# Performance work log

Measured on AMD Instinct MI355X. Metric: run time of the kernel, lower is better.

The kernel has to match this reference:

```python
import jax, jax.numpy as jnp
import numpy as np

N, E, D_IN, D_H, D_OUT = 100000, 1600000, 128, 128, 47
BN_EPS = 1e-5


def setup_inputs() -> dict:
    key = jax.random.key(0)
    ks = jax.random.split(key, 12)
    x = jax.random.normal(ks[0], (N, D_IN), dtype=jnp.float32)
    edge_index = jax.random.randint(ks[1], (2, E), 0, N, dtype=jnp.int64)
    s = 1.0 / np.sqrt(D_H)
    return {
        "x": x,
        "edge_index": edge_index,
        "W1": jax.random.normal(ks[2], (D_IN, D_H), dtype=jnp.float32) * s,
        "b1": jnp.zeros((D_H,), dtype=jnp.float32),
        "gamma": jax.random.uniform(ks[3], (D_H,), dtype=jnp.float32, minval=0.5, maxval=1.5),
        "beta": jax.random.normal(ks[4], (D_H,), dtype=jnp.float32) * 0.1,
        "mean": jax.random.normal(ks[5], (D_H,), dtype=jnp.float32) * 0.1,
        "var": jax.random.uniform(ks[6], (D_H,), dtype=jnp.float32, minval=0.5, maxval=1.5),
        "W2": jax.random.normal(ks[7], (D_H, D_H), dtype=jnp.float32) * s,
        "b2": jnp.zeros((D_H,), dtype=jnp.float32),
        "Wf": jax.random.normal(ks[8], (D_H, D_OUT), dtype=jnp.float32) * s,
        "bf": jnp.zeros((D_OUT,), dtype=jnp.float32),
    }


def gcn_conv(x, src, dst, W, b, n):
    # x' = x @ W, then symmetric-normalized aggregation with self-loops (PyG GCNConv).
    h = x @ W
    loops = jnp.arange(n, dtype=src.dtype)
    s = jnp.concatenate([src, loops])
    d = jnp.concatenate([dst, loops])
    deg = jax.ops.segment_sum(jnp.ones_like(d, dtype=h.dtype), d, num_segments=n)
    dinv = jnp.where(deg > 0, jax.lax.rsqrt(deg), 0.0)
    norm = dinv[s] * dinv[d]                      # [E+N]
    msg = h[s] * norm[:, None]                    # [E+N, D] gather
    out = jax.ops.segment_sum(msg, d, num_segments=n)  # scatter-add
    return out + b


def reference(x, edge_index, W1, b1, gamma, beta, mean, var, W2, b2, Wf, bf):
    n = x.shape[0]
    src, dst = edge_index[0], edge_index[1]
    # layer 1: GCNConv -> BatchNorm (eval) -> ReLU -> dropout (identity in eval)
    h1 = gcn_conv(x, src, dst, W1, b1, n)
    h1 = (h1 - mean) * jax.lax.rsqrt(var + BN_EPS) * gamma + beta
    h1 = jax.nn.relu(h1)
    # layer 2 (last conv, no BN/act)
    h2 = gcn_conv(h1, src, dst, W2, b2, n)
    # JumpingKnowledge max over layer outputs
    jk = jnp.maximum(h1, h2)
    logits = jk @ Wf + bf
    return jax.nn.log_softmax(logits, axis=1)
```

## Files before the change

kernel.cpp:

```cpp
#include <hip/hip_runtime.h>
#include <math.h>

#define DH 128
#define DOUT 47
#define BN_EPS 1e-5f

typedef __attribute__((ext_vector_type(8))) short short8;
typedef __attribute__((ext_vector_type(4))) float float4v;
typedef __attribute__((ext_vector_type(2))) float float2v;

__device__ __forceinline__ unsigned bf16_rne(float f) {
    unsigned u = __float_as_uint(f);
    return (u + 0x7fffu + ((u >> 16) & 1u)) >> 16;
}
__device__ __forceinline__ unsigned pack_bf2(float a, float b) {
    return (bf16_rne(a) & 0xffffu) | (bf16_rne(b) << 16);
}
__device__ __forceinline__ float2 unpack_bf2(unsigned u) {
    return make_float2(__uint_as_float(u << 16),
                       __uint_as_float(u & 0xffff0000u));
}


__global__ __launch_bounds__(256) void prep_k(const float* __restrict__ W1,
                                              const float* __restrict__ W2,
                                              unsigned* __restrict__ W1b,
                                              unsigned* __restrict__ W2b,
                                              int* __restrict__ counts8,
                                              unsigned* __restrict__ bufA, int n) {
    int tid = threadIdx.x;
    if (blockIdx.x >= 2) {
        int i4 = (blockIdx.x - 2) * 256 + tid;
        if (i4 < n * 2) *(int4*)(counts8 + (size_t)i4 * 4) = make_int4(0, 0, 0, 0);
        return;
    }
    const float* W = blockIdx.x ? W2 : W1;
    unsigned* Wb = blockIdx.x ? W2b : W1b;
    if (blockIdx.x == 0 && tid < 64) bufA[(size_t)n * 64 + tid] = 0;
    for (int p = tid; p < 128 * 32; p += 256) {
        int nn = p >> 5;
        int k0 = (p & 31) << 2;
        float f0 = W[(size_t)(k0 + 0) * 128 + nn];
        float f1 = W[(size_t)(k0 + 1) * 128 + nn];
        float f2 = W[(size_t)(k0 + 2) * 128 + nn];
        float f3 = W[(size_t)(k0 + 3) * 128 + nn];
        uint2 v;
        v.x = pack_bf2(f0, f1);
        v.y = pack_bf2(f2, f3);
        *(uint2*)(Wb + (size_t)nn * 64 + (k0 >> 1)) = v;
    }
}

__device__ __forceinline__ int xcc_id() {
    int x;
    asm volatile("s_getreg_b32 %0, hwreg(HW_REG_XCC_ID)" : "=s"(x));
    return x & 7;
}

__global__ __launch_bounds__(256) void fused_gc_k(
    const float* __restrict__ A, const unsigned* __restrict__ Wb,
    unsigned* __restrict__ Cb, int M,
    const int* __restrict__ dst, int* __restrict__ counts8,
    int* __restrict__ rank, int e, int gemmBlocks, int n) {
    __shared__ ushort Bl[128 * 136];
    int bid = blockIdx.x;
    int r3 = bid % 3;
    int q3 = bid / 3;
    int tid = threadIdx.x;

    if (r3 == 2) {
        int xcc = xcc_id();
        int* cnt = counts8 + (size_t)xcc * n;
        int tag = xcc << 24;
        int i0 = (q3 * 256 + tid) * 8;
#define CADD(d) ((int)__hip_atomic_fetch_add(&cnt[(d)], 1, __ATOMIC_RELAXED, \
                                             __HIP_MEMORY_SCOPE_WORKGROUP) | tag)
        if (i0 + 8 <= e) {
            int4 d4 = *(const int4*)(dst + i0);
            int4 e4 = *(const int4*)(dst + i0 + 4);
            int4 r4, s4;
            r4.x = CADD(d4.x);
            r4.y = CADD(d4.y);
            r4.z = CADD(d4.z);
            r4.w = CADD(d4.w);
            s4.x = CADD(e4.x);
            s4.y = CADD(e4.y);
            s4.z = CADD(e4.z);
            s4.w = CADD(e4.w);
            *(int4*)(rank + i0) = r4;
            *(int4*)(rank + i0 + 4) = s4;
        } else {
            for (int i = i0; i < e; i++) rank[i] = CADD(dst[i]);
        }
#undef CADD
        return;
    }

    int gIdx = q3 * 2 + r3;
    if (gIdx >= gemmBlocks) return;
    {
        unsigned* Bu = (unsigned*)Bl;
        for (int q = tid; q < 128 * 16; q += 256) {
            int row = q >> 4;
            int c = (q & 15) << 2;
            uint4 v = *(const uint4*)(Wb + (size_t)row * 64 + c);
            *(uint4*)(Bu + (size_t)row * 68 + c) = v;
        }
    }
    __syncthreads();

    int lane = tid & 63;
    int wv = tid >> 6;
    int quad = lane >> 4;
    int l15 = lane & 15;
    int r0 = gIdx * 64 + wv * 16;
    int mload = r0 + l15;
    if (mload > M - 1) mload = M - 1;
    const float* Ar = A + (size_t)mload * 128 + quad * 8;

    float4v acc[8];
#pragma unroll
    for (int t = 0; t < 8; t++) acc[t] = (float4v){0.f, 0.f, 0.f, 0.f};

    for (int kp = 0; kp < 4; ++kp) {
        float4 a0 = *(const float4*)(Ar + kp * 32);
        float4 a1 = *(const float4*)(Ar + kp * 32 + 4);
        float af[8] = {a0.x, a0.y, a0.z, a0.w, a1.x, a1.y, a1.z, a1.w};
        short8 av;
#pragma unroll
        for (int j = 0; j < 8; j++) av[j] = (short)bf16_rne(af[j]);
        int kb = kp * 32 + quad * 8;
#pragma unroll
        for (int nt = 0; nt < 8; nt++) {
            short8 b8 = *(const short8*)(&Bl[(size_t)(nt * 16 + l15) * 136 + kb]);
            acc[nt] = __builtin_amdgcn_mfma_f32_16x16x32_bf16(av, b8, acc[nt], 0, 0, 0);
        }
    }

    ushort* Cu = (ushort*)Cb;
#pragma unroll
    for (int r = 0; r < 4; r++) {
        int row = r0 + quad * 4 + r;
        if (row < M) {
#pragma unroll
            for (int nt = 0; nt < 8; nt++) {
                Cu[(size_t)row * 128 + nt * 16 + l15] =
                    (ushort)bf16_rne(acc[nt][r]);
            }
        }
    }
}

__global__ __launch_bounds__(256) void scan1_k(const int* __restrict__ counts8,
                                               int* __restrict__ offsets,
                                               int* __restrict__ blocksums, int n) {
    __shared__ int sd[256];
    int tid = threadIdx.x;
    int base = blockIdx.x * 1024 + tid * 4;
    int v[4];
#pragma unroll
    for (int j = 0; j < 4; j++) {
        int idx = base + j;
        int c = 0;
        if (idx < n) {
#pragma unroll
            for (int r = 0; r < 8; r++) c += counts8[(size_t)r * n + idx];
            c = (c + 7) & ~7;
        }
        v[j] = c;
    }
    int tsum = v[0] + v[1] + v[2] + v[3];
    sd[tid] = tsum;
    __syncthreads();
    for (int off = 1; off < 256; off <<= 1) {
        int x = (tid >= off) ? sd[tid - off] : 0;
        __syncthreads();
        sd[tid] += x;
        __syncthreads();
    }
    if (tid == 255) blocksums[blockIdx.x] = sd[255];
    int run = sd[tid] - tsum;
    if (base + 0 < n) offsets[base + 0] = run;  run += v[0];
    if (base + 1 < n) offsets[base + 1] = run;  run += v[1];
    if (base + 2 < n) offsets[base + 2] = run;  run += v[2];
    if (base + 3 < n) offsets[base + 3] = run;
}

__global__ __launch_bounds__(128) void scan2_k(int* __restrict__ blocksums, int nb,
                                               int* __restrict__ el, int n) {
    __shared__ int sd[128];
    int tid = threadIdx.x;
    int v = (tid < nb) ? blocksums[tid] : 0;
    sd[tid] = v;
    __syncthreads();
    for (int off = 1; off < 128; off <<= 1) {
        int x = (tid >= off) ? sd[tid - off] : 0;
        __syncthreads();
        sd[tid] += x;
        __syncthreads();
    }
    if (tid < nb) blocksums[tid] = sd[tid] - v;
    int total = sd[127];
    if (tid < 96) el[total + tid] = n;
}

__global__ void finalize_k(int* __restrict__ offsets,
                           float* __restrict__ dinv, int* __restrict__ counts8,
                           const int* __restrict__ blocksums,
                           int* __restrict__ base8,
                           int* __restrict__ el, int n) {
    int i = blockIdx.x * 256 + threadIdx.x;
    if (i >= n) return;
    int o = offsets[i] + blocksums[i >> 10];
    offsets[i] = o;
    int run = o;
#pragma unroll
    for (int r = 0; r < 8; r++) {
        base8[(size_t)i * 8 + r] = run;
        run += counts8[(size_t)r * n + i];
    }
    int c = run - o;
    counts8[i] = c;
    dinv[i] = rsqrtf((float)(c + 1));
    int cP = (c + 7) & ~7;
    for (int j = o + c; j < o + cP; ++j) el[j] = n;
}

__global__ __launch_bounds__(256) void scatter_k(const int* __restrict__ src,
                                                 const int* __restrict__ dst,
                                                 const int* __restrict__ rank,
                                                 const int* __restrict__ base8,
                                                 const float* __restrict__ dinv,
                                                 int* __restrict__ el, int e) {
    int i0 = (blockIdx.x * 256 + threadIdx.x) * 4;
    if (i0 + 4 <= e) {
        int4 s4 = *(const int4*)(src + i0);
        int4 d4 = *(const int4*)(dst + i0);
        int4 r4 = *(const int4*)(rank + i0);
        unsigned qx = (unsigned)(dinv[s4.x] * 32767.f + 0.5f);
        unsigned qy = (unsigned)(dinv[s4.y] * 32767.f + 0.5f);
        unsigned qz = (unsigned)(dinv[s4.z] * 32767.f + 0.5f);
        unsigned qw = (unsigned)(dinv[s4.w] * 32767.f + 0.5f);
        int ix = base8[(size_t)d4.x * 8 + (((unsigned)r4.x >> 24) & 7)] + (r4.x & 0xFFFFFF);
        int iy = base8[(size_t)d4.y * 8 + (((unsigned)r4.y >> 24) & 7)] + (r4.y & 0xFFFFFF);
        int iz = base8[(size_t)d4.z * 8 + (((unsigned)r4.z >> 24) & 7)] + (r4.z & 0xFFFFFF);
        int iw = base8[(size_t)d4.w * 8 + (((unsigned)r4.w >> 24) & 7)] + (r4.w & 0xFFFFFF);
        el[ix] = (int)((unsigned)s4.x | (qx << 17));
        el[iy] = (int)((unsigned)s4.y | (qy << 17));
        el[iz] = (int)((unsigned)s4.z | (qz << 17));
        el[iw] = (int)((unsigned)s4.w | (qw << 17));
    } else {
        for (int i = i0; i < e; i++) {
            unsigned q = (unsigned)(dinv[src[i]] * 32767.f + 0.5f);
            int rw = rank[i];
            int idx = base8[(size_t)dst[i] * 8 + (((unsigned)rw >> 24) & 7)] + (rw & 0xFFFFFF);
            el[idx] = (int)((unsigned)src[i] | (q << 17));
        }
    }
}

__global__ __launch_bounds__(256) void gemm_bf16_k(const unsigned* __restrict__ Ab,
                                                   const unsigned* __restrict__ Wb,
                                                   unsigned* __restrict__ Cb, int M) {
    __shared__ ushort Bl[128 * 136];
    int tid = threadIdx.x;
    {
        unsigned* Bu = (unsigned*)Bl;
        for (int q = tid; q < 128 * 16; q += 256) {
            int row = q >> 4;
            int c = (q & 15) << 2;
            uint4 v = *(const uint4*)(Wb + (size_t)row * 64 + c);
            *(uint4*)(Bu + (size_t)row * 68 + c) = v;
        }
    }
    __syncthreads();

    int lane = tid & 63;
    int wv = tid >> 6;
    int quad = lane >> 4;
    int l15 = lane & 15;
    int r0 = blockIdx.x * 64 + wv * 16;
    int mload = r0 + l15;
    if (mload > M - 1) mload = M - 1;
    const unsigned* Ar = Ab + (size_t)mload * 64 + quad * 4;

    float4v acc[8];
#pragma unroll
    for (int t = 0; t < 8; t++) acc[t] = (float4v){0.f, 0.f, 0.f, 0.f};

    for (int kp = 0; kp < 4; ++kp) {
        uint4 a4 = *(const uint4*)(Ar + kp * 16);
        short8 av;
        av[0] = (short)(a4.x & 0xffff); av[1] = (short)(a4.x >> 16);
        av[2] = (short)(a4.y & 0xffff); av[3] = (short)(a4.y >> 16);
        av[4] = (short)(a4.z & 0xffff); av[5] = (short)(a4.z >> 16);
        av[6] = (short)(a4.w & 0xffff); av[7] = (short)(a4.w >> 16);
        int kb = kp * 32 + quad * 8;
#pragma unroll
        for (int nt = 0; nt < 8; nt++) {
            short8 b8 = *(const short8*)(&Bl[(size_t)(nt * 16 + l15) * 136 + kb]);
            acc[nt] = __builtin_amdgcn_mfma_f32_16x16x32_bf16(av, b8, acc[nt], 0, 0, 0);
        }
    }

    ushort* Cu = (ushort*)Cb;
#pragma unroll
    for (int r = 0; r < 4; r++) {
        int row = r0 + quad * 4 + r;
        if (row < M) {
#pragma unroll
            for (int nt = 0; nt < 8; nt++) {
                Cu[(size_t)row * 128 + nt * 16 + l15] =
                    (ushort)bf16_rne(acc[nt][r]);
            }
        }
    }
}

__device__ __forceinline__ float4 agg_core(const uint2* __restrict__ Hu2,
                                           const int* __restrict__ el,
                                           int start, int cnt, int node,
                                           float dvn, int li, int half) {
    float2v a01 = {0.f, 0.f};
    float2v a23 = {0.f, 0.f};
    int groups = ((cnt + 7) & ~7) >> 3;
    if (groups > 0) {
        const int* p = el + start + half * 4;

#define EDGE(cu, rr) {                                                       \
        float qf = (float)((unsigned)(rr) >> 17) * (1.f / 32767.f);          \
        float2v f0, f1;                                                      \
        f0.x = __uint_as_float((cu).x << 16);                                \
        f0.y = __uint_as_float((cu).x & 0xffff0000u);                        \
        f1.x = __uint_as_float((cu).y << 16);                                \
        f1.y = __uint_as_float((cu).y & 0xffff0000u);                        \
        a01.x = fmaf(f0.x, qf, a01.x); a01.y = fmaf(f0.y, qf, a01.y);        \
        a23.x = fmaf(f1.x, qf, a23.x); a23.y = fmaf(f1.y, qf, a23.y);        \
}
        int4 rc = *(const int4*)p;
        uint2 c0 = Hu2[(size_t)(rc.x & 0x1FFFF) * 32 + li];
        uint2 c1 = Hu2[(size_t)(rc.y & 0x1FFFF) * 32 + li];
        uint2 c2 = Hu2[(size_t)(rc.z & 0x1FFFF) * 32 + li];
        uint2 c3 = Hu2[(size_t)(rc.w & 0x1FFFF) * 32 + li];
        int4 rn = *(const int4*)(p + 8);
        for (int g = 0; g < groups; ++g) {
            uint2 n0 = Hu2[(size_t)(rn.x & 0x1FFFF) * 32 + li];
            uint2 n1 = Hu2[(size_t)(rn.y & 0x1FFFF) * 32 + li];
            uint2 n2 = Hu2[(size_t)(rn.z & 0x1FFFF) * 32 + li];
            uint2 n3 = Hu2[(size_t)(rn.w & 0x1FFFF) * 32 + li];
            int4 r2 = *(const int4*)(p + 8 * (g + 2));
            EDGE(c0, rc.x) EDGE(c1, rc.y) EDGE(c2, rc.z) EDGE(c3, rc.w)
            c0 = n0; c1 = n1; c2 = n2; c3 = n3;
            rc = rn; rn = r2;
        }
#undef EDGE
    }
    float4 acc = make_float4(a01.x, a01.y, a23.x, a23.y);
    acc.x += __shfl_xor(acc.x, 32);
    acc.y += __shfl_xor(acc.y, 32);
    acc.z += __shfl_xor(acc.z, 32);
    acc.w += __shfl_xor(acc.w, 32);
    uint2 sv = Hu2[(size_t)node * 32 + li];
    float2 s0 = unpack_bf2(sv.x);
    float2 s1 = unpack_bf2(sv.y);
    acc.x = fmaf(s0.x, dvn, acc.x); acc.y = fmaf(s0.y, dvn, acc.y);
    acc.z = fmaf(s1.x, dvn, acc.z); acc.w = fmaf(s1.y, dvn, acc.w);
    return acc;
}

__global__ __launch_bounds__(256) void agg1_k(
    const unsigned* __restrict__ H, const int* __restrict__ el,
    const int* __restrict__ offsets, const int* __restrict__ counts,
    const float* __restrict__ dinv, const float* __restrict__ b1,
    const float* __restrict__ gamma, const float* __restrict__ beta,
    const float* __restrict__ mean, const float* __restrict__ var,
    unsigned* __restrict__ H1b, int n) {
    int lane = threadIdx.x & 63;
    int li = lane & 31;
    int half = lane >> 5;
    int node = blockIdx.x * 4 + (threadIdx.x >> 6);
    if (node >= n) return;
    float dv = dinv[node];
    float4 acc = agg_core((const uint2*)H, el, offsets[node],
                          counts[node], node, dv, li, half);
    if (half == 0) {
        int f0 = li * 4;
        float4 bb = *(const float4*)(b1 + f0);
        float4 mm = *(const float4*)(mean + f0);
        float4 vv = *(const float4*)(var + f0);
        float4 gg = *(const float4*)(gamma + f0);
        float4 be = *(const float4*)(beta + f0);
        float4 o;
        o.x = fmaxf((acc.x * dv + bb.x - mm.x) * rsqrtf(vv.x + BN_EPS) * gg.x + be.x, 0.f);
        o.y = fmaxf((acc.y * dv + bb.y - mm.y) * rsqrtf(vv.y + BN_EPS) * gg.y + be.y, 0.f);
        o.z = fmaxf((acc.z * dv + bb.z - mm.z) * rsqrtf(vv.z + BN_EPS) * gg.z + be.z, 0.f);
        o.w = fmaxf((acc.w * dv + bb.w - mm.w) * rsqrtf(vv.w + BN_EPS) * gg.w + be.w, 0.f);
        uint2 pk;
        pk.x = pack_bf2(o.x, o.y);
        pk.y = pack_bf2(o.z, o.w);
        *(uint2*)(H1b + (size_t)node * 64 + li * 2) = pk;
    }
}

__global__ __launch_bounds__(256) void agg2_k(
    const unsigned* __restrict__ H, const int* __restrict__ el,
    const int* __restrict__ offsets, const int* __restrict__ counts,
    const float* __restrict__ dinv, const float* __restrict__ b2,
    unsigned* __restrict__ H1b, int n) {
    int lane = threadIdx.x & 63;
    int li = lane & 31;
    int half = lane >> 5;
    int node = blockIdx.x * 4 + (threadIdx.x >> 6);
    if (node >= n) return;
    float dv = dinv[node];
    float4 acc = agg_core((const uint2*)H, el, offsets[node],
                          counts[node], node, dv, li, half);
    if (half == 0) {
        int f0 = li * 4;
        float4 bb = *(const float4*)(b2 + f0);
        uint2* p = (uint2*)(H1b + (size_t)node * 64 + li * 2);
        uint2 hv = *p;
        float2 ha = unpack_bf2(hv.x);
        float2 hb = unpack_bf2(hv.y);
        float4 o;
        o.x = fmaxf(ha.x, acc.x * dv + bb.x);
        o.y = fmaxf(ha.y, acc.y * dv + bb.y);
        o.z = fmaxf(hb.x, acc.z * dv + bb.z);
        o.w = fmaxf(hb.y, acc.w * dv + bb.w);
        uint2 pk;
        pk.x = pack_bf2(o.x, o.y);
        pk.y = pack_bf2(o.z, o.w);
        *p = pk;
    }
}

__global__ __launch_bounds__(256) void head_k(const unsigned* __restrict__ JKb,
                                              const float* __restrict__ Wf,
                                              const float* __restrict__ bf,
                                              float* __restrict__ out, int n) {
    __shared__ __align__(16) float Bs[48 * 132];
    __shared__ __align__(16) float As[64 * 36];
    int tid = threadIdx.x;
    for (int p = tid; p < 47 * 32; p += 256) {
        int c = p >> 5;
        int k0 = (p & 31) << 2;
        float4 v;
        v.x = Wf[(size_t)(k0 + 0) * DOUT + c];
        v.y = Wf[(size_t)(k0 + 1) * DOUT + c];
        v.z = Wf[(size_t)(k0 + 2) * DOUT + c];
        v.w = Wf[(size_t)(k0 + 3) * DOUT + c];
        *(float4*)(&Bs[c * 132 + k0]) = v;
    }
    int tx = tid & 15;
    int ty = tid >> 4;
    int node0 = blockIdx.x * 64;

    float acc[4][3];
#pragma unroll
    for (int i = 0; i < 4; i++)
#pragma unroll
        for (int j = 0; j < 3; j++) acc[i][j] = 0.f;

    for (int kk = 0; kk < 128; kk += 32) {
        __syncthreads();
        for (int l = tid; l < 512; l += 256) {
            int r = l >> 3;
            int c4 = (l & 7) << 2;
            int row = node0 + r;
            float4 v = make_float4(0.f, 0.f, 0.f, 0.f);
            if (row < n) {
                uint2 u = *(const uint2*)(JKb + (size_t)row * 64 + ((kk + c4) >> 1));
                float2 f0 = unpack_bf2(u.x);
                float2 f1 = unpack_bf2(u.y);
                v = make_float4(f0.x, f0.y, f1.x, f1.y);
            }
            *(float4*)(&As[r * 36 + c4]) = v;
        }
        __syncthreads();
#pragma unroll
        for (int k4 = 0; k4 < 32; k4 += 4) {
            float4 a0 = *(const float4*)(&As[(ty * 4 + 0) * 36 + k4]);
            float4 a1 = *(const float4*)(&As[(ty * 4 + 1) * 36 + k4]);
            float4 a2 = *(const float4*)(&As[(ty * 4 + 2) * 36 + k4]);
            float4 a3 = *(const float4*)(&As[(ty * 4 + 3) * 36 + k4]);
            float4 b0 = *(const float4*)(&Bs[(tx * 3 + 0) * 132 + kk + k4]);
            float4 b1 = *(const float4*)(&Bs[(tx * 3 + 1) * 132 + kk + k4]);
            float4 b2 = *(const float4*)(&Bs[(tx * 3 + 2) * 132 + kk + k4]);
#define DOT_ROW(i, a)                                                        \
            acc[i][0] = fmaf(a.x, b0.x, acc[i][0]);                          \
            acc[i][0] = fmaf(a.y, b0.y, acc[i][0]);                          \
            acc[i][0] = fmaf(a.z, b0.z, acc[i][0]);                          \
            acc[i][0] = fmaf(a.w, b0.w, acc[i][0]);                          \
            acc[i][1] = fmaf(a.x, b1.x, acc[i][1]);                          \
            acc[i][1] = fmaf(a.y, b1.y, acc[i][1]);                          \
            acc[i][1] = fmaf(a.z, b1.z, acc[i][1]);                          \
            acc[i][1] = fmaf(a.w, b1.w, acc[i][1]);                          \
            acc[i][2] = fmaf(a.x, b2.x, acc[i][2]);                          \
            acc[i][2] = fmaf(a.y, b2.y, acc[i][2]);                          \
            acc[i][2] = fmaf(a.z, b2.z, acc[i][2]);                          \
            acc[i][2] = fmaf(a.w, b2.w, acc[i][2]);
            DOT_ROW(0, a0)
            DOT_ROW(1, a1)
            DOT_ROW(2, a2)
            DOT_ROW(3, a3)
#undef DOT_ROW
        }
    }

    float bfv[3];
#pragma unroll
    for (int j = 0; j < 3; j++) {
        int c = tx * 3 + j;
        bfv[j] = (c < DOUT) ? bf[c] : 0.f;
    }
#pragma unroll
    for (int i = 0; i < 4; i++) {
        int node = node0 + ty * 4 + i;
        float l0 = acc[i][0] + bfv[0];
        float l1 = acc[i][1] + bfv[1];
        float l2 = acc[i][2] + bfv[2];
        bool v2ok = (tx * 3 + 2) < DOUT;
        float m = fmaxf(l0, l1);
        if (v2ok) m = fmaxf(m, l2);
        for (int off = 8; off >= 1; off >>= 1) m = fmaxf(m, __shfl_xor(m, off));
        float s = expf(l0 - m) + expf(l1 - m) + (v2ok ? expf(l2 - m) : 0.f);
        for (int off = 8; off >= 1; off >>= 1) s += __shfl_xor(s, off);
        float ls = m + logf(s);
        if (node < n) {
            float* o = out + (size_t)node * DOUT + tx * 3;
            o[0] = l0 - ls;
            o[1] = l1 - ls;
            if (v2ok) o[2] = l2 - ls;
        }
    }
}

extern "C" void kernel_launch(void* const* d_in, const int* in_sizes, int n_in,
                              void* d_out, int out_size, void* d_ws, size_t ws_size,
                              hipStream_t stream) {
    const float* x     = (const float*)d_in[0];
    const int*   ei    = (const int*)d_in[1];
    const float* W1    = (const float*)d_in[2];
    const float* b1    = (const float*)d_in[3];
    const float* gamma = (const float*)d_in[4];
    const float* beta  = (const float*)d_in[5];
    const float* mean  = (const float*)d_in[6];
    const float* var   = (const float*)d_in[7];
    const float* W2    = (const float*)d_in[8];
    const float* b2    = (const float*)d_in[9];
    const float* Wf    = (const float*)d_in[10];
    const float* bf    = (const float*)d_in[11];
    float* out = (float*)d_out;

    int N_ = in_sizes[0] / 128;
    int E_ = in_sizes[1] / 2;
    const int* src = ei;
    const int* dst = ei + E_;

    char* ws = (char*)d_ws;
    unsigned* bufA = (unsigned*)ws; ws += (size_t)(N_ + 1) * 64 * 4;
    unsigned* h1b  = (unsigned*)ws; ws += (size_t)N_ * 64 * 4;
    int* counts8   = (int*)ws;    ws += (size_t)N_ * 8 * 4;
    int* base8     = (int*)ws;    ws += (size_t)N_ * 8 * 4;
    int*   offsets = (int*)ws;    ws += (size_t)N_ * 4;
    float* dinv    = (float*)ws;  ws += (size_t)N_ * 4;
    int*   rank    = (int*)ws;    ws += (size_t)E_ * 4;
    int*   el      = (int*)ws;    ws += ((size_t)E_ + 7 * (size_t)N_ + 128) * 4;
    int*   bsums   = (int*)ws;    ws += 1024 * 4;
    unsigned* W1b  = (unsigned*)ws; ws += 128 * 64 * 4;
    unsigned* W2b  = (unsigned*)ws; ws += 128 * 64 * 4;

    int nb = (N_ + 1023) / 1024;
    int gemmBlocks = (N_ + 63) / 64;
    int countBlocks = (E_ + 2047) / 2048;
    int pairs = countBlocks > (gemmBlocks + 1) / 2 ? countBlocks : (gemmBlocks + 1) / 2;
    int fusedGrid = 3 * pairs;
    int edgeBlocks = (E_ + 1023) / 1024;
    int zeroBlocks = (N_ * 2 + 255) / 256;

    prep_k<<<2 + zeroBlocks, 256, 0, stream>>>(W1, W2, W1b, W2b, counts8, bufA, N_);
    fused_gc_k<<<fusedGrid, 256, 0, stream>>>(x, W1b, bufA, N_,
                                              dst, counts8, rank, E_, gemmBlocks, N_);
    scan1_k<<<nb, 256, 0, stream>>>(counts8, offsets, bsums, N_);
    scan2_k<<<1, 128, 0, stream>>>(bsums, nb, el, N_);
    finalize_k<<<(N_ + 255) / 256, 256, 0, stream>>>(offsets, dinv,
                                                     counts8, bsums, base8, el, N_);
    scatter_k<<<edgeBlocks, 256, 0, stream>>>(src, dst, rank, base8, dinv, el, E_);

    agg1_k<<<(N_ + 3) / 4, 256, 0, stream>>>(bufA, el, offsets, counts8, dinv,
                                             b1, gamma, beta, mean, var, h1b, N_);
    gemm_bf16_k<<<gemmBlocks, 256, 0, stream>>>(h1b, W2b, bufA, N_);
    agg2_k<<<(N_ + 3) / 4, 256, 0, stream>>>(bufA, el, offsets, counts8, dinv,
                                             b2, h1b, N_);
    head_k<<<(N_ + 63) / 64, 256, 0, stream>>>(h1b, Wf, bf, out, N_);
}
```

Baseline: 420.4 us.

## Replace global atomic degree counting with LDS-bin chunked histogram and fuse scatter with GEMM

Degree counting and per-edge ranking now run in a dedicated kernel that keeps a 32K-node range of bins in shared memory for each of 64 edge chunks, using LDS atomics instead of per-XCC global atomics. Per-chunk counts are reduced in the scan and turned into per-chunk base offsets in finalize, with the per-chunk count buffer aliased onto the h1 buffer. The first feature GEMM is moved out of the counting kernel and fused with the edge scatter kernel. This trades global atomic traffic for one more read pass over dst per node range and a larger 64-way reduction in scan and finalize.

```diff
diff --git a/kernel.cpp b/kernel.cpp
--- a/kernel.cpp
+++ b/kernel.cpp
@@ -4,6 +4,10 @@
 #define DH 128
 #define DOUT 47
 #define BN_EPS 1e-5f
+
+#define NCH 64
+#define RS 32768
+#define RSH 15
 
 typedef __attribute__((ext_vector_type(8))) short short8;
 typedef __attribute__((ext_vector_type(4))) float float4v;
@@ -26,14 +30,8 @@
                                               const float* __restrict__ W2,
                                               unsigned* __restrict__ W1b,
                                               unsigned* __restrict__ W2b,
-                                              int* __restrict__ counts8,
                                               unsigned* __restrict__ bufA, int n) {
     int tid = threadIdx.x;
-    if (blockIdx.x >= 2) {
-        int i4 = (blockIdx.x - 2) * 256 + tid;
-        if (i4 < n * 2) *(int4*)(counts8 + (size_t)i4 * 4) = make_int4(0, 0, 0, 0);
-        return;
-    }
     const float* W = blockIdx.x ? W2 : W1;
     unsigned* Wb = blockIdx.x ? W2b : W1b;
     if (blockIdx.x == 0 && tid < 64) bufA[(size_t)n * 64 + tid] = 0;
@@ -51,109 +49,51 @@
     }
 }
 
-__device__ __forceinline__ int xcc_id() {
-    int x;
-    asm volatile("s_getreg_b32 %0, hwreg(HW_REG_XCC_ID)" : "=s"(x));
-    return x & 7;
-}
-
-__global__ __launch_bounds__(256) void fused_gc_k(
-    const float* __restrict__ A, const unsigned* __restrict__ Wb,
-    unsigned* __restrict__ Cb, int M,
-    const int* __restrict__ dst, int* __restrict__ counts8,
-    int* __restrict__ rank, int e, int gemmBlocks, int n) {
-    __shared__ ushort Bl[128 * 136];
-    int bid = blockIdx.x;
-    int r3 = bid % 3;
-    int q3 = bid / 3;
-    int tid = threadIdx.x;
-
-    if (r3 == 2) {
-        int xcc = xcc_id();
-        int* cnt = counts8 + (size_t)xcc * n;
-        int tag = xcc << 24;
-        int i0 = (q3 * 256 + tid) * 8;
-#define CADD(d) ((int)__hip_atomic_fetch_add(&cnt[(d)], 1, __ATOMIC_RELAXED, \
-                                             __HIP_MEMORY_SCOPE_WORKGROUP) | tag)
-        if (i0 + 8 <= e) {
+__global__ __launch_bounds__(256) void hist_rank_k(const int* __restrict__ dst,
+                                                   int* __restrict__ rank,
+                                                   int* __restrict__ cntM,
+                                                   int e, int ce, int nr,
+                                                   size_t nsp) {
+    __shared__ int bins[RS];
+    int tid = threadIdx.x;
+    int r = blockIdx.x % nr;
+    int ch = blockIdx.x / nr;
+    {
+        int4* b4 = (int4*)bins;
+        for (int j = tid; j < RS / 4; j += 256) b4[j] = make_int4(0, 0, 0, 0);
+    }
+    __syncthreads();
+    int lo = ch * ce;
+    int hi = lo + ce;
+    if (hi > e) hi = e;
+    if (lo < hi) {
+        int n4end = lo + ((hi - lo) & ~3);
+        for (int i0 = lo + tid * 4; i0 < n4end; i0 += 1024) {
             int4 d4 = *(const int4*)(dst + i0);
-            int4 e4 = *(const int4*)(dst + i0 + 4);
-            int4 r4, s4;
-            r4.x = CADD(d4.x);
-            r4.y = CADD(d4.y);
-            r4.z = CADD(d4.z);
-            r4.w = CADD(d4.w);
-            s4.x = CADD(e4.x);
-            s4.y = CADD(e4.y);
-            s4.z = CADD(e4.z);
-            s4.w = CADD(e4.w);
-            *(int4*)(rank + i0) = r4;
-            *(int4*)(rank + i0 + 4) = s4;
-        } else {
-            for (int i = i0; i < e; i++) rank[i] = CADD(dst[i]);
-        }
-#undef CADD
-        return;
-    }
-
-    int gIdx = q3 * 2 + r3;
-    if (gIdx >= gemmBlocks) return;
+            if ((d4.x >> RSH) == r) rank[i0 + 0] = atomicAdd(&bins[d4.x & (RS - 1)], 1);
+            if ((d4.y >> RSH) == r) rank[i0 + 1] = atomicAdd(&bins[d4.y & (RS - 1)], 1);
+            if ((d4.z >> RSH) == r) rank[i0 + 2] = atomicAdd(&bins[d4.z & (RS - 1)], 1);
+            if ((d4.w >> RSH) == r) rank[i0 + 3] = atomicAdd(&bins[d4.w & (RS - 1)], 1);
+        }
+        for (int i0 = n4end + tid; i0 < hi; i0 += 256) {
+            int d = dst[i0];
+            if ((d >> RSH) == r) rank[i0] = atomicAdd(&bins[d & (RS - 1)], 1);
+        }
+    }
+    __syncthreads();
     {
-        unsigned* Bu = (unsigned*)Bl;
-        for (int q = tid; q < 128 * 16; q += 256) {
-            int row = q >> 4;
-            int c = (q & 15) << 2;
-            uint4 v = *(const uint4*)(Wb + (size_t)row * 64 + c);
-            *(uint4*)(Bu + (size_t)row * 68 + c) = v;
-        }
-    }
-    __syncthreads();
-
-    int lane = tid & 63;
-    int wv = tid >> 6;
-    int quad = lane >> 4;
-    int l15 = lane & 15;
-    int r0 = gIdx * 64 + wv * 16;
-    int mload = r0 + l15;
-    if (mload > M - 1) mload = M - 1;
-    const float* Ar = A + (size_t)mload * 128 + quad * 8;
-
-    float4v acc[8];
-#pragma unroll
-    for (int t = 0; t < 8; t++) acc[t] = (float4v){0.f, 0.f, 0.f, 0.f};
-
-    for (int kp = 0; kp < 4; ++kp) {
-        float4 a0 = *(const float4*)(Ar + kp * 32);
-        float4 a1 = *(const float4*)(Ar + kp * 32 + 4);
-        float af[8] = {a0.x, a0.y, a0.z, a0.w, a1.x, a1.y, a1.z, a1.w};
-        short8 av;
-#pragma unroll
-        for (int j = 0; j < 8; j++) av[j] = (short)bf16_rne(af[j]);
-        int kb = kp * 32 + quad * 8;
-#pragma unroll
-        for (int nt = 0; nt < 8; nt++) {
-            short8 b8 = *(const short8*)(&Bl[(size_t)(nt * 16 + l15) * 136 + kb]);
-            acc[nt] = __builtin_amdgcn_mfma_f32_16x16x32_bf16(av, b8, acc[nt], 0, 0, 0);
-        }
-    }
-
-    ushort* Cu = (ushort*)Cb;
-#pragma unroll
-    for (int r = 0; r < 4; r++) {
-        int row = r0 + quad * 4 + r;
-        if (row < M) {
-#pragma unroll
-            for (int nt = 0; nt < 8; nt++) {
-                Cu[(size_t)row * 128 + nt * 16 + l15] =
-                    (ushort)bf16_rne(acc[nt][r]);
-            }
-        }
-    }
-}
-
-__global__ __launch_bounds__(256) void scan1_k(const int* __restrict__ counts8,
+        int* outp = cntM + (size_t)ch * nsp + ((size_t)r << RSH);
+        const int4* b4 = (const int4*)bins;
+        int4* o4 = (int4*)outp;
+        for (int j = tid; j < RS / 4; j += 256) o4[j] = b4[j];
+    }
+}
+
+__global__ __launch_bounds__(256) void scan1_k(const int* __restrict__ cntM,
+                                               int* __restrict__ counts,
                                                int* __restrict__ offsets,
-                                               int* __restrict__ blocksums, int n) {
+                                               int* __restrict__ blocksums,
+                                               size_t nsp, int n) {
     __shared__ int sd[256];
     int tid = threadIdx.x;
     int base = blockIdx.x * 1024 + tid * 4;
@@ -163,8 +103,8 @@
         int idx = base + j;
         int c = 0;
         if (idx < n) {
-#pragma unroll
-            for (int r = 0; r < 8; r++) c += counts8[(size_t)r * n + idx];
+            for (int ch = 0; ch < NCH; ch++) c += cntM[(size_t)ch * nsp + idx];
+            counts[idx] = c;
             c = (c + 7) & ~7;
         }
         v[j] = c;
@@ -205,56 +145,115 @@
 }
 
 __global__ void finalize_k(int* __restrict__ offsets,
-                           float* __restrict__ dinv, int* __restrict__ counts8,
+                           float* __restrict__ dinv,
+                           const int* __restrict__ counts,
                            const int* __restrict__ blocksums,
-                           int* __restrict__ base8,
-                           int* __restrict__ el, int n) {
+                           int* __restrict__ cntM,
+                           int* __restrict__ el, size_t nsp, int n) {
     int i = blockIdx.x * 256 + threadIdx.x;
     if (i >= n) return;
     int o = offsets[i] + blocksums[i >> 10];
     offsets[i] = o;
     int run = o;
-#pragma unroll
-    for (int r = 0; r < 8; r++) {
-        base8[(size_t)i * 8 + r] = run;
-        run += counts8[(size_t)r * n + i];
-    }
-    int c = run - o;
-    counts8[i] = c;
+    for (int ch = 0; ch < NCH; ch++) {
+        size_t idx = (size_t)ch * nsp + i;
+        int c = cntM[idx];
+        cntM[idx] = run;
+        run += c;
+    }
+    int c = counts[i];
     dinv[i] = rsqrtf((float)(c + 1));
     int cP = (c + 7) & ~7;
     for (int j = o + c; j < o + cP; ++j) el[j] = n;
 }
 
-__global__ __launch_bounds__(256) void scatter_k(const int* __restrict__ src,
-                                                 const int* __restrict__ dst,
-                                                 const int* __restrict__ rank,
-                                                 const int* __restrict__ base8,
-                                                 const float* __restrict__ dinv,
-                                                 int* __restrict__ el, int e) {
-    int i0 = (blockIdx.x * 256 + threadIdx.x) * 4;
-    if (i0 + 4 <= e) {
-        int4 s4 = *(const int4*)(src + i0);
-        int4 d4 = *(const int4*)(dst + i0);
-        int4 r4 = *(const int4*)(rank + i0);
-        unsigned qx = (unsigned)(dinv[s4.x] * 32767.f + 0.5f);
-        unsigned qy = (unsigned)(dinv[s4.y] * 32767.f + 0.5f);
-        unsigned qz = (unsigned)(dinv[s4.z] * 32767.f + 0.5f);
-        unsigned qw = (unsigned)(dinv[s4.w] * 32767.f + 0.5f);
-        int ix = base8[(size_t)d4.x * 8 + (((unsigned)r4.x >> 24) & 7)] + (r4.x & 0xFFFFFF);
-        int iy = base8[(size_t)d4.y * 8 + (((unsigned)r4.y >> 24) & 7)] + (r4.y & 0xFFFFFF);
-        int iz = base8[(size_t)d4.z * 8 + (((unsigned)r4.z >> 24) & 7)] + (r4.z & 0xFFFFFF);
-        int iw = base8[(size_t)d4.w * 8 + (((unsigned)r4.w >> 24) & 7)] + (r4.w & 0xFFFFFF);
-        el[ix] = (int)((unsigned)s4.x | (qx << 17));
-        el[iy] = (int)((unsigned)s4.y | (qy << 17));
-        el[iz] = (int)((unsigned)s4.z | (qz << 17));
-        el[iw] = (int)((unsigned)s4.w | (qw << 17));
-    } else {
-        for (int i = i0; i < e; i++) {
-            unsigned q = (unsigned)(dinv[src[i]] * 32767.f + 0.5f);
-            int rw = rank[i];
-            int idx = base8[(size_t)dst[i] * 8 + (((unsigned)rw >> 24) & 7)] + (rw & 0xFFFFFF);
-            el[idx] = (int)((unsigned)src[i] | (q << 17));
+__global__ __launch_bounds__(256) void fused_sg_k(
+    const float* __restrict__ A, const unsigned* __restrict__ Wb,
+    unsigned* __restrict__ Cb, int M,
+    const int* __restrict__ src, const int* __restrict__ dst,
+    const int* __restrict__ rank, const int* __restrict__ baseM,
+    const float* __restrict__ dinv, int* __restrict__ el,
+    int e, int ce, size_t nsp, int gemmBlocks) {
+    __shared__ ushort Bl[128 * 136];
+    int bid = blockIdx.x;
+    int q = bid >> 1;
+    int tid = threadIdx.x;
+
+    if (bid & 1) {
+        int i0 = (q * 256 + tid) * 4;
+        if (i0 + 4 <= e) {
+            int4 s4 = *(const int4*)(src + i0);
+            int4 d4 = *(const int4*)(dst + i0);
+            int4 r4 = *(const int4*)(rank + i0);
+            const int* bM = baseM + (size_t)(i0 / ce) * nsp;
+            unsigned qx = (unsigned)(dinv[s4.x] * 32767.f + 0.5f);
+            unsigned qy = (unsigned)(dinv[s4.y] * 32767.f + 0.5f);
+            unsigned qz = (unsigned)(dinv[s4.z] * 32767.f + 0.5f);
+            unsigned qw = (unsigned)(dinv[s4.w] * 32767.f + 0.5f);
+            el[bM[d4.x] + r4.x] = (int)((unsigned)s4.x | (qx << 17));
+            el[bM[d4.y] + r4.y] = (int)((unsigned)s4.y | (qy << 17));
+            el[bM[d4.z] + r4.z] = (int)((unsigned)s4.z | (qz << 17));
+            el[bM[d4.w] + r4.w] = (int)((unsigned)s4.w | (qw << 17));
+        } else {
+            for (int i = i0; i < e; i++) {
+                unsigned qv = (unsigned)(dinv[src[i]] * 32767.f + 0.5f);
+                int idx = baseM[(size_t)(i / ce) * nsp + dst[i]] + rank[i];
+                el[idx] = (int)((unsigned)src[i] | (qv << 17));
+            }
+        }
+        return;
+    }
+
+    if (q >= gemmBlocks) return;
+    {
+        unsigned* Bu = (unsigned*)Bl;
+        for (int p = tid; p < 128 * 16; p += 256) {
+            int row = p >> 4;
+            int c = (p & 15) << 2;
+            uint4 v = *(const uint4*)(Wb + (size_t)row * 64 + c);
+            *(uint4*)(Bu + (size_t)row * 68 + c) = v;
+        }
+    }
+    __syncthreads();
+
+    int lane = tid & 63;
+    int wv = tid >> 6;
+    int quad = lane >> 4;
+    int l15 = lane & 15;
+    int r0 = q * 64 + wv * 16;
+    int mload = r0 + l15;
+    if (mload > M - 1) mload = M - 1;
+    const float* Ar = A + (size_t)mload * 128 + quad * 8;
+
+    float4v acc[8];
+#pragma unroll
+    for (int t = 0; t < 8; t++) acc[t] = (float4v){0.f, 0.f, 0.f, 0.f};
+
+    for (int kp = 0; kp < 4; ++kp) {
+        float4 a0 = *(const float4*)(Ar + kp * 32);
+        float4 a1 = *(const float4*)(Ar + kp * 32 + 4);
+        float af[8] = {a0.x, a0.y, a0.z, a0.w, a1.x, a1.y, a1.z, a1.w};
+        short8 av;
+#pragma unroll
+        for (int j = 0; j < 8; j++) av[j] = (short)bf16_rne(af[j]);
+        int kb = kp * 32 + quad * 8;
+#pragma unroll
+        for (int nt = 0; nt < 8; nt++) {
+            short8 b8 = *(const short8*)(&Bl[(size_t)(nt * 16 + l15) * 136 + kb]);
+            acc[nt] = __builtin_amdgcn_mfma_f32_16x16x32_bf16(av, b8, acc[nt], 0, 0, 0);
+        }
+    }
+
+    ushort* Cu = (ushort*)Cb;
+#pragma unroll
+    for (int r = 0; r < 4; r++) {
+        int row = r0 + quad * 4 + r;
+        if (row < M) {
+#pragma unroll
+            for (int nt = 0; nt < 8; nt++) {
+                Cu[(size_t)row * 128 + nt * 16 + l15] =
+                    (ushort)bf16_rne(acc[nt][r]);
+            }
         }
     }
 }
@@ -557,11 +556,17 @@
     const int* src = ei;
     const int* dst = ei + E_;
 
+    int NR = (N_ + RS - 1) >> RSH;
+    size_t NSP = (size_t)NR << RSH;
+    int CE = ((E_ + NCH - 1) / NCH + 3) & ~3;
+
     char* ws = (char*)d_ws;
     unsigned* bufA = (unsigned*)ws; ws += (size_t)(N_ + 1) * 64 * 4;
-    unsigned* h1b  = (unsigned*)ws; ws += (size_t)N_ * 64 * 4;
-    int* counts8   = (int*)ws;    ws += (size_t)N_ * 8 * 4;
-    int* base8     = (int*)ws;    ws += (size_t)N_ * 8 * 4;
+    size_t h1bSz = (size_t)N_ * 64 * 4;
+    size_t cntSz = (size_t)NCH * NSP * 4;
+    unsigned* h1b = (unsigned*)ws;
+    int* cntM     = (int*)ws;       ws += (h1bSz > cntSz ? h1bSz : cntSz);
+    int*   counts  = (int*)ws;    ws += (size_t)N_ * 4;
     int*   offsets = (int*)ws;    ws += (size_t)N_ * 4;
     float* dinv    = (float*)ws;  ws += (size_t)N_ * 4;
     int*   rank    = (int*)ws;    ws += (size_t)E_ * 4;
@@ -572,25 +577,22 @@
 
     int nb = (N_ + 1023) / 1024;
     int gemmBlocks = (N_ + 63) / 64;
-    int countBlocks = (E_ + 2047) / 2048;
-    int pairs = countBlocks > (gemmBlocks + 1) / 2 ? countBlocks : (gemmBlocks + 1) / 2;
-    int fusedGrid = 3 * pairs;
-    int edgeBlocks = (E_ + 1023) / 1024;
-    int zeroBlocks = (N_ * 2 + 255) / 256;
-
-    prep_k<<<2 + zeroBlocks, 256, 0, stream>>>(W1, W2, W1b, W2b, counts8, bufA, N_);
-    fused_gc_k<<<fusedGrid, 256, 0, stream>>>(x, W1b, bufA, N_,
-                                              dst, counts8, rank, E_, gemmBlocks, N_);
-    scan1_k<<<nb, 256, 0, stream>>>(counts8, offsets, bsums, N_);
+    int scatBlocks = (E_ + 1023) / 1024;
+    int pairs = gemmBlocks > scatBlocks ? gemmBlocks : scatBlocks;
+
+    prep_k<<<2, 256, 0, stream>>>(W1, W2, W1b, W2b, bufA, N_);
+    hist_rank_k<<<NCH * NR, 256, 0, stream>>>(dst, rank, cntM, E_, CE, NR, NSP);
+    scan1_k<<<nb, 256, 0, stream>>>(cntM, counts, offsets, bsums, NSP, N_);
     scan2_k<<<1, 128, 0, stream>>>(bsums, nb, el, N_);
-    finalize_k<<<(N_ + 255) / 256, 256, 0, stream>>>(offsets, dinv,
-                                                     counts8, bsums, base8, el, N_);
-    scatter_k<<<edgeBlocks, 256, 0, stream>>>(src, dst, rank, base8, dinv, el, E_);
-
-    agg1_k<<<(N_ + 3) / 4, 256, 0, stream>>>(bufA, el, offsets, counts8, dinv,
+    finalize_k<<<(N_ + 255) / 256, 256, 0, stream>>>(offsets, dinv, counts,
+                                                     bsums, cntM, el, NSP, N_);
+    fused_sg_k<<<2 * pairs, 256, 0, stream>>>(x, W1b, bufA, N_,
+                                              src, dst, rank, cntM, dinv, el,
+                                              E_, CE, NSP, gemmBlocks);
+    agg1_k<<<(N_ + 3) / 4, 256, 0, stream>>>(bufA, el, offsets, counts, dinv,
                                              b1, gamma, beta, mean, var, h1b, N_);
     gemm_bf16_k<<<gemmBlocks, 256, 0, stream>>>(h1b, W2b, bufA, N_);
-    agg2_k<<<(N_ + 3) / 4, 256, 0, stream>>>(bufA, el, offsets, counts8, dinv,
+    agg2_k<<<(N_ + 3) / 4, 256, 0, stream>>>(bufA, el, offsets, counts, dinv,
                                              b2, h1b, N_);
     head_k<<<(N_ + 63) / 64, 256, 0, stream>>>(h1b, Wf, bf, out, N_);
 }
```

Result: no change. 415.8 us (-1.1%).
